# Kernel tuning notes

Measured on AMD Instinct MI355X. Metric: run time of the kernel, lower is better.

Reference implementation:

```python
import jax, jax.numpy as jnp
import numpy as np

N, S, D_MODEL, H = 2, 2048, 1024, 16
HEAD_DIM = D_MODEL // H


def setup_inputs() -> dict:
    key = jax.random.key(0)
    k1, k2, k3 = jax.random.split(key, 3)
    x = jax.random.normal(k1, (N, S, D_MODEL), dtype=jnp.float32)
    # Xavier-uniform-like scaling for the projection weights (torch layout: [out, in])
    lim_qkv = (6.0 / (D_MODEL + 3 * D_MODEL)) ** 0.5
    lim_o = (6.0 / (D_MODEL + D_MODEL)) ** 0.5
    qkv_w = jax.random.uniform(k2, (3 * D_MODEL, D_MODEL), dtype=jnp.float32, minval=-lim_qkv, maxval=lim_qkv)
    o_w = jax.random.uniform(k3, (D_MODEL, D_MODEL), dtype=jnp.float32, minval=-lim_o, maxval=lim_o)
    return {"x": x, "qkv_w": qkv_w, "o_w": o_w}


def reference(x, qkv_w, o_w):
    n, s, _ = x.shape
    # qkv projection (torch Linear: y = x @ W^T), no bias
    qkv = jnp.einsum("nsd,ed->nse", x, qkv_w)            # (N, S, 3*D_MODEL)
    qkv = qkv.reshape(n, s, H, 3 * HEAD_DIM).transpose(0, 2, 1, 3)  # (N, H, S, 3*hd)
    q, k, v = jnp.split(qkv, 3, axis=-1)                 # each (N, H, S, hd)
    scale = 1.0 / jnp.sqrt(jnp.float32(HEAD_DIM))
    attn_logits = jnp.einsum("nhqd,nhkd->nhqk", q, k) * scale  # (N, H, S, S)
    attn_weights = jax.nn.softmax(attn_logits, axis=-1)
    values = jnp.einsum("nhqk,nhkd->nhqd", attn_weights, v)    # (N, H, S, hd)
    values = values.transpose(0, 2, 1, 3).reshape(n, s, D_MODEL)
    o = jnp.einsum("nsd,ed->nse", values, o_w)           # (N, S, D_MODEL)
    return o
```

## Files before the change

kernel.cpp:

```cpp
#include <hip/hip_runtime.h>
#include <math.h>

#define H 16
#define S 2048
#define DM 1024
#define HD 64
#define QSCALE 0.18033688011112042f

typedef __attribute__((ext_vector_type(8))) short short8;
typedef __attribute__((ext_vector_type(4))) float f32x4;
typedef __attribute__((ext_vector_type(4))) unsigned short u16x4;
typedef __attribute__((ext_vector_type(2))) unsigned int uint2v;
#if __has_builtin(__builtin_amdgcn_cvt_pk_bf16_f32)
typedef __attribute__((ext_vector_type(2))) __bf16 bf16x2;
#endif

__device__ __forceinline__ unsigned short f2bf(float f) {
  unsigned int u = __builtin_bit_cast(unsigned int, f);
  u = (u + 0x7fffu + ((u >> 16) & 1u)) >> 16;
  return (unsigned short)u;
}

__device__ __forceinline__ unsigned int pk_bf16(float a, float b) {
#if __has_builtin(__builtin_amdgcn_cvt_pk_bf16_f32)
  bf16x2 r = __builtin_amdgcn_cvt_pk_bf16_f32(a, b);
  return __builtin_bit_cast(unsigned int, r);
#else
  return (unsigned int)f2bf(a) | ((unsigned int)f2bf(b) << 16);
#endif
}

__device__ __forceinline__ float fexp2(float x) {
#if __has_builtin(__builtin_amdgcn_exp2f)
  return __builtin_amdgcn_exp2f(x);
#else
  return exp2f(x);
#endif
}

__device__ __forceinline__ void async_ld16(const void* g, void* l) {
  __builtin_amdgcn_global_load_lds(
      (const __attribute__((address_space(1))) unsigned int*)g,
      (__attribute__((address_space(3))) unsigned int*)l, 16, 0, 0);
}

__global__ void convert_all(const float* __restrict__ x, const float* __restrict__ w,
                            const float* __restrict__ ow,
                            unsigned short* __restrict__ xb,
                            unsigned short* __restrict__ wb,
                            unsigned short* __restrict__ owb) {
  int b = blockIdx.x;
  const f32x4* src;
  u16x4* dst;
  int idx;
  if (b < 4096) {
    src = (const f32x4*)x; dst = (u16x4*)xb; idx = b * 256 + threadIdx.x;
  } else if (b < 7168) {
    src = (const f32x4*)w; dst = (u16x4*)wb; idx = (b - 4096) * 256 + threadIdx.x;
  } else {
    src = (const f32x4*)ow; dst = (u16x4*)owb; idx = (b - 7168) * 256 + threadIdx.x;
  }
  f32x4 v = src[idx];
  u16x4 r;
  r.x = f2bf(v.x); r.y = f2bf(v.y); r.z = f2bf(v.z); r.w = f2bf(v.w);
  dst[idx] = r;
}

__global__ __launch_bounds__(256, 3) void gemm_qkv(
    const short* __restrict__ X, const short* __restrict__ W,
    unsigned short* __restrict__ qws, unsigned short* __restrict__ kws,
    unsigned short* __restrict__ vtws) {
  const int K = 1024;
  __shared__ __attribute__((aligned(16))) short As[128 * 64];
  __shared__ __attribute__((aligned(16))) short Bs[128 * 64];
  const int tid = threadIdx.x;
  const int w = tid >> 6, l = tid & 63, l15 = l & 15, quad = l >> 4;
  const int wm = (w >> 1) * 64, wn = (w & 1) * 64;
  const int row0 = blockIdx.y * 128, col0 = blockIdx.x * 128;

  f32x4 zero = {0.f, 0.f, 0.f, 0.f};
  f32x4 acc[4][4];
  for (int i = 0; i < 4; ++i)
    for (int j = 0; j < 4; ++j) acc[i][j] = zero;

  const short* Ag = X + row0 * K;
  const short* Bg = W + col0 * K;

  const int rs = l15 & 7;

  for (int k0 = 0; k0 < K; k0 += 64) {
    __syncthreads();
    for (int i = 0; i < 4; ++i) {
      int u = i * 256 + tid;
      int r = u >> 3, c = (u & 7) ^ (r & 7);
      async_ld16(Ag + r * K + k0 + c * 8, As + u * 8);
    }
    for (int i = 0; i < 4; ++i) {
      int u = i * 256 + tid;
      int r = u >> 3, c = (u & 7) ^ (r & 7);
      async_ld16(Bg + r * K + k0 + c * 8, Bs + u * 8);
    }
    __syncthreads();
    for (int kk = 0; kk < 2; ++kk) {
      const int slot = ((kk * 4 + quad) ^ rs) * 8;
      short8 a[4], b[4];
      for (int i = 0; i < 4; ++i)
        a[i] = *(const short8*)(As + (wm + i * 16 + l15) * 64 + slot);
      for (int j = 0; j < 4; ++j)
        b[j] = *(const short8*)(Bs + (wn + j * 16 + l15) * 64 + slot);
      for (int i = 0; i < 4; ++i)
        for (int j = 0; j < 4; ++j)
          acc[i][j] = __builtin_amdgcn_mfma_f32_16x16x32_bf16(a[i], b[j], acc[i][j], 0, 0, 0);
    }
  }

  for (int i = 0; i < 4; ++i) {
    int rowb = row0 + wm + i * 16 + quad * 4;
    int n = rowb >> 11, s = rowb & 2047;
    for (int j = 0; j < 4; ++j) {
      int e = col0 + wn + j * 16 + l15;
      int h = e / 192;
      int rem = e - h * 192;
      int part = rem >> 6, d = rem & 63;
      f32x4 v = acc[i][j];
      if (part == 0) {
        unsigned short* p = qws + ((n * H + h) * S + s) * HD + d;
        p[0] = f2bf(v.x * QSCALE);
        p[HD] = f2bf(v.y * QSCALE);
        p[2 * HD] = f2bf(v.z * QSCALE);
        p[3 * HD] = f2bf(v.w * QSCALE);
      } else if (part == 1) {
        unsigned short* p = kws + ((n * H + h) * S + s) * HD + d;
        p[0] = f2bf(v.x);
        p[HD] = f2bf(v.y);
        p[2 * HD] = f2bf(v.z);
        p[3 * HD] = f2bf(v.w);
      } else {
        u16x4 pk;
        pk.x = f2bf(v.x); pk.y = f2bf(v.y); pk.z = f2bf(v.z); pk.w = f2bf(v.w);
        *(u16x4*)(vtws + ((n * H + h) * HD + d) * S + s) = pk;
      }
    }
  }
}

__global__ __launch_bounds__(512, 4) void flash(
    const short* __restrict__ qws, const short* __restrict__ kws,
    const short* __restrict__ vtws, unsigned short* __restrict__ vals) {
  __shared__ __attribute__((aligned(16))) short Ks[2][128 * 64];
  __shared__ __attribute__((aligned(16))) short Vts[2][2][64 * 64];
  __shared__ __attribute__((aligned(16))) short Pt[8][16 * 64];
  const int tid = threadIdx.x;
  const int w = tid >> 6, l = tid & 63, l15 = l & 15, quad = l >> 4;
  const int b = blockIdx.x;
  const int hn = (b & 7) * 4 + (b >> 7);
  const int qb = (b >> 3) & 15;
  const int h = hn & 15, n = hn >> 4;
  const int nh = n * H + h;
  const short* Qh = qws + nh * S * HD;
  const short* Kh = kws + nh * S * HD;
  const short* Vth = vtws + nh * HD * S;

  const int q0 = qb * 128 + w * 16;
  short8 qf[2];
  for (int c = 0; c < 2; ++c)
    qf[c] = *(const short8*)(Qh + (q0 + l15) * HD + c * 32 + quad * 8);

  const int swz0 = ((4 * 0 + quad) ^ (l15 & 7)) * 8;
  const int swz1 = ((4 * 1 + quad) ^ (l15 & 7)) * 8;

  float lpart = 0.f;
  f32x4 zero = {0.f, 0.f, 0.f, 0.f};
  f32x4 oacc[4] = {zero, zero, zero, zero};

  auto stage = [&](int kv0, int buf) {
    for (int i = 0; i < 2; ++i) {
      int u = i * 512 + tid;
      int r = u >> 3;
      int c = (u & 7) ^ (r & 7);
      async_ld16(Kh + (kv0 + r) * HD + c * 8, &Ks[buf][u * 8]);
    }
    for (int i = 0; i < 2; ++i) {
      int v = tid;
      int r = v >> 3;
      int c = (v & 7) ^ (r & 7);
      async_ld16(Vth + r * S + kv0 + i * 64 + c * 8, &Vts[buf][i][v * 8]);
    }
  };

  stage(0, 0);
  for (int t = 0; t < 16; ++t) {
    const int buf = t & 1;
    __syncthreads();
    if (t < 15) stage((t + 1) * 128, buf ^ 1);

    for (int ss = 0; ss < 2; ++ss) {
      const short* Kb = &Ks[buf][ss * 64 * 64];
      const short* Vb = Vts[buf][ss];

      f32x4 sacc[4] = {zero, zero, zero, zero};
      {
        short8 kf[4];
        for (int i = 0; i < 4; ++i)
          kf[i] = *(const short8*)(Kb + (i * 16 + l15) * 64 + swz0);
        for (int i = 0; i < 4; ++i)
          sacc[i] = __builtin_amdgcn_mfma_f32_16x16x32_bf16(kf[i], qf[0], sacc[i], 0, 0, 0);
        for (int i = 0; i < 4; ++i)
          kf[i] = *(const short8*)(Kb + (i * 16 + l15) * 64 + swz1);
        for (int i = 0; i < 4; ++i)
          sacc[i] = __builtin_amdgcn_mfma_f32_16x16x32_bf16(kf[i], qf[1], sacc[i], 0, 0, 0);
      }

      for (int i = 0; i < 4; ++i) {
        f32x4 p;
        p.x = fexp2(sacc[i].x);
        p.y = fexp2(sacc[i].y);
        p.z = fexp2(sacc[i].z);
        p.w = fexp2(sacc[i].w);
        sacc[i] = p;
        lpart += p.x + p.y + p.z + p.w;
      }

      for (int i = 0; i < 4; ++i) {
        int g = 2 * i + (quad >> 1);
        uint2v pk;
        pk.x = pk_bf16(sacc[i].x, sacc[i].y);
        pk.y = pk_bf16(sacc[i].z, sacc[i].w);
        *(uint2v*)(&Pt[w][l15 * 64 + ((g ^ (l15 & 7)) * 8) + (quad & 1) * 4]) = pk;
      }
      asm volatile("s_waitcnt lgkmcnt(0)" ::: "memory");

      {
        short8 vf[4];
        short8 pf0 = *(const short8*)(&Pt[w][l15 * 64 + swz0]);
        short8 pf1 = *(const short8*)(&Pt[w][l15 * 64 + swz1]);
        for (int i = 0; i < 4; ++i)
          vf[i] = *(const short8*)(Vb + (i * 16 + l15) * 64 + swz0);
        for (int i = 0; i < 4; ++i)
          oacc[i] = __builtin_amdgcn_mfma_f32_16x16x32_bf16(vf[i], pf0, oacc[i], 0, 0, 0);
        for (int i = 0; i < 4; ++i)
          vf[i] = *(const short8*)(Vb + (i * 16 + l15) * 64 + swz1);
        for (int i = 0; i < 4; ++i)
          oacc[i] = __builtin_amdgcn_mfma_f32_16x16x32_bf16(vf[i], pf1, oacc[i], 0, 0, 0);
      }
    }
  }

  float lrun = lpart;
  lrun += __shfl_xor(lrun, 16);
  lrun += __shfl_xor(lrun, 32);
  float inv = 1.0f / lrun;
  int s = q0 + l15;
  for (int i = 0; i < 4; ++i) {
    uint2v pk;
    pk.x = pk_bf16(oacc[i].x * inv, oacc[i].y * inv);
    pk.y = pk_bf16(oacc[i].z * inv, oacc[i].w * inv);
    *(uint2v*)(vals + (n * S + s) * DM + h * HD + i * 16 + quad * 4) = pk;
  }
}

__global__ __launch_bounds__(256, 2) void gemm_out(
    const short* __restrict__ A, const short* __restrict__ W,
    float* __restrict__ out) {
  const int K = 1024;
  __shared__ __attribute__((aligned(16))) short As[128 * 64];
  __shared__ __attribute__((aligned(16))) short Bs[64 * 64];
  const int tid = threadIdx.x;
  const int w = tid >> 6, l = tid & 63, l15 = l & 15, quad = l >> 4;
  const int wm = (w >> 1) * 64, wn = (w & 1) * 32;
  const int row0 = blockIdx.y * 128, col0 = blockIdx.x * 64;

  f32x4 zero = {0.f, 0.f, 0.f, 0.f};
  f32x4 acc[4][2];
  for (int i = 0; i < 4; ++i)
    for (int j = 0; j < 2; ++j) acc[i][j] = zero;

  const short* Ag = A + row0 * K;
  const short* Bg = W + col0 * K;

  const int rs = l15 & 7;

  for (int k0 = 0; k0 < K; k0 += 64) {
    __syncthreads();
    for (int i = 0; i < 4; ++i) {
      int u = i * 256 + tid;
      int r = u >> 3, c = (u & 7) ^ (r & 7);
      async_ld16(Ag + r * K + k0 + c * 8, As + u * 8);
    }
    for (int i = 0; i < 2; ++i) {
      int u = i * 256 + tid;
      int r = u >> 3, c = (u & 7) ^ (r & 7);
      async_ld16(Bg + r * K + k0 + c * 8, Bs + u * 8);
    }
    __syncthreads();
    for (int kk = 0; kk < 2; ++kk) {
      const int slot = ((kk * 4 + quad) ^ rs) * 8;
      short8 a[4], b[2];
      for (int i = 0; i < 4; ++i)
        a[i] = *(const short8*)(As + (wm + i * 16 + l15) * 64 + slot);
      for (int j = 0; j < 2; ++j)
        b[j] = *(const short8*)(Bs + (wn + j * 16 + l15) * 64 + slot);
      for (int i = 0; i < 4; ++i)
        for (int j = 0; j < 2; ++j)
          acc[i][j] = __builtin_amdgcn_mfma_f32_16x16x32_bf16(a[i], b[j], acc[i][j], 0, 0, 0);
    }
  }

  for (int i = 0; i < 4; ++i) {
    int rowb = row0 + wm + i * 16 + quad * 4;
    for (int j = 0; j < 2; ++j) {
      int e = col0 + wn + j * 16 + l15;
      f32x4 v = acc[i][j];
      out[(rowb + 0) * 1024 + e] = v.x;
      out[(rowb + 1) * 1024 + e] = v.y;
      out[(rowb + 2) * 1024 + e] = v.z;
      out[(rowb + 3) * 1024 + e] = v.w;
    }
  }
}

extern "C" void kernel_launch(void* const* d_in, const int* in_sizes, int n_in,
                              void* d_out, int out_size, void* d_ws, size_t ws_size,
                              hipStream_t stream) {
  const float* x = (const float*)d_in[0];
  const float* qkv_w = (const float*)d_in[1];
  const float* o_w = (const float*)d_in[2];
  float* out = (float*)d_out;

  char* ws = (char*)d_ws;
  unsigned short* xb   = (unsigned short*)(ws);
  unsigned short* wb   = (unsigned short*)(ws + (8ull << 20));
  unsigned short* owb  = (unsigned short*)(ws + (14ull << 20));
  unsigned short* qws  = (unsigned short*)(ws + (16ull << 20));
  unsigned short* kws  = (unsigned short*)(ws + (24ull << 20));
  unsigned short* vtws = (unsigned short*)(ws + (32ull << 20));
  unsigned short* vals = xb;

  convert_all<<<8192, 256, 0, stream>>>(x, qkv_w, o_w, xb, wb, owb);
  gemm_qkv<<<dim3(24, 32), 256, 0, stream>>>(
      (const short*)xb, (const short*)wb, qws, kws, vtws);
  flash<<<512, 512, 0, stream>>>(
      (const short*)qws, (const short*)kws, (const short*)vtws, vals);
  gemm_out<<<dim3(16, 32), 256, 0, stream>>>(
      (const short*)vals, (const short*)owb, out);
}
```

Before: 180.6 us.

## Permute K rows so P fragments feed PV MFMA directly from registers

New measurement: 171.5 us. 1.05x faster.

```diff
diff --git a/kernel.cpp b/kernel.cpp
--- a/kernel.cpp
+++ b/kernel.cpp
@@ -11,6 +11,7 @@
 typedef __attribute__((ext_vector_type(4))) float f32x4;
 typedef __attribute__((ext_vector_type(4))) unsigned short u16x4;
 typedef __attribute__((ext_vector_type(2))) unsigned int uint2v;
+typedef __attribute__((ext_vector_type(4))) unsigned int uint4v;
 #if __has_builtin(__builtin_amdgcn_cvt_pk_bf16_f32)
 typedef __attribute__((ext_vector_type(2))) __bf16 bf16x2;
 #endif
@@ -149,7 +150,6 @@
     const short* __restrict__ vtws, unsigned short* __restrict__ vals) {
   __shared__ __attribute__((aligned(16))) short Ks[2][128 * 64];
   __shared__ __attribute__((aligned(16))) short Vts[2][2][64 * 64];
-  __shared__ __attribute__((aligned(16))) short Pt[8][16 * 64];
   const int tid = threadIdx.x;
   const int w = tid >> 6, l = tid & 63, l15 = l & 15, quad = l >> 4;
   const int b = blockIdx.x;
@@ -168,6 +168,7 @@
 
   const int swz0 = ((4 * 0 + quad) ^ (l15 & 7)) * 8;
   const int swz1 = ((4 * 1 + quad) ^ (l15 & 7)) * 8;
+  const int rbase = 8 * (l15 >> 2) + (l15 & 3);
 
   float lpart = 0.f;
   f32x4 zero = {0.f, 0.f, 0.f, 0.f};
@@ -177,7 +178,7 @@
     for (int i = 0; i < 2; ++i) {
       int u = i * 512 + tid;
       int r = u >> 3;
-      int c = (u & 7) ^ (r & 7);
+      int c = (u & 7) ^ ((r & 3) | (((r >> 3) & 1) << 2));
       async_ld16(Kh + (kv0 + r) * HD + c * 8, &Ks[buf][u * 8]);
     }
     for (int i = 0; i < 2; ++i) {
@@ -202,11 +203,11 @@
       {
         short8 kf[4];
         for (int i = 0; i < 4; ++i)
-          kf[i] = *(const short8*)(Kb + (i * 16 + l15) * 64 + swz0);
+          kf[i] = *(const short8*)(Kb + (rbase + 4 * (i & 1) + 32 * (i >> 1)) * 64 + swz0);
         for (int i = 0; i < 4; ++i)
           sacc[i] = __builtin_amdgcn_mfma_f32_16x16x32_bf16(kf[i], qf[0], sacc[i], 0, 0, 0);
         for (int i = 0; i < 4; ++i)
-          kf[i] = *(const short8*)(Kb + (i * 16 + l15) * 64 + swz1);
+          kf[i] = *(const short8*)(Kb + (rbase + 4 * (i & 1) + 32 * (i >> 1)) * 64 + swz1);
         for (int i = 0; i < 4; ++i)
           sacc[i] = __builtin_amdgcn_mfma_f32_16x16x32_bf16(kf[i], qf[1], sacc[i], 0, 0, 0);
       }
@@ -221,19 +222,20 @@
         lpart += p.x + p.y + p.z + p.w;
       }
 
-      for (int i = 0; i < 4; ++i) {
-        int g = 2 * i + (quad >> 1);
-        uint2v pk;
-        pk.x = pk_bf16(sacc[i].x, sacc[i].y);
-        pk.y = pk_bf16(sacc[i].z, sacc[i].w);
-        *(uint2v*)(&Pt[w][l15 * 64 + ((g ^ (l15 & 7)) * 8) + (quad & 1) * 4]) = pk;
-      }
-      asm volatile("s_waitcnt lgkmcnt(0)" ::: "memory");
+      uint4v w0, w1;
+      w0.x = pk_bf16(sacc[0].x, sacc[0].y);
+      w0.y = pk_bf16(sacc[0].z, sacc[0].w);
+      w0.z = pk_bf16(sacc[1].x, sacc[1].y);
+      w0.w = pk_bf16(sacc[1].z, sacc[1].w);
+      w1.x = pk_bf16(sacc[2].x, sacc[2].y);
+      w1.y = pk_bf16(sacc[2].z, sacc[2].w);
+      w1.z = pk_bf16(sacc[3].x, sacc[3].y);
+      w1.w = pk_bf16(sacc[3].z, sacc[3].w);
+      short8 pf0 = __builtin_bit_cast(short8, w0);
+      short8 pf1 = __builtin_bit_cast(short8, w1);
 
       {
         short8 vf[4];
-        short8 pf0 = *(const short8*)(&Pt[w][l15 * 64 + swz0]);
-        short8 pf1 = *(const short8*)(&Pt[w][l15 * 64 + swz1]);
         for (int i = 0; i < 4; ++i)
           vf[i] = *(const short8*)(Vb + (i * 16 + l15) * 64 + swz0);
         for (int i = 0; i < 4; ++i)
```
